# Kernel tuning notes

Measured on AMD Instinct MI355X. Metric: run time of the kernel, lower is better.

Reference implementation:

```python
import jax, jax.numpy as jnp
import numpy as np

B, S, D, H = 2, 2048, 2048, 16
HD = D // H
RESIDUAL_SCALE = 1.0
EPS = 1e-6


def setup_inputs() -> dict:
    key = jax.random.key(0)
    ks = jax.random.split(key, 6)
    x = jax.random.normal(ks[0], (B, S, D), jnp.float32)
    # rotary tables: emb = cat(freqs, freqs), shape [S, HD]
    inv_freq = 1.0 / (10000.0 ** (jnp.arange(0, HD, 2, dtype=jnp.float32) / HD))
    t = jnp.arange(S, dtype=jnp.float32)
    freqs = jnp.einsum('s,f->sf', t, inv_freq)
    emb = jnp.concatenate([freqs, freqs], axis=-1)
    cos, sin = jnp.cos(emb), jnp.sin(emb)
    sc = 0.02
    w_qkv = jax.random.normal(ks[1], (3 * D, D), jnp.float32) * sc
    w_out = jax.random.normal(ks[2], (D, D), jnp.float32) * sc
    w_fc1 = jax.random.normal(ks[3], (4 * D, D), jnp.float32) * sc
    w_fc2 = jax.random.normal(ks[4], (D, 4 * D), jnp.float32) * sc
    g1 = jnp.ones((D,), jnp.float32)
    g2 = jnp.ones((D,), jnp.float32)
    return {'x': x, 'cos': cos, 'sin': sin, 'g1': g1, 'g2': g2,
            'w_qkv': w_qkv, 'w_out': w_out, 'w_fc1': w_fc1, 'w_fc2': w_fc2}


def _rmsnorm(x, g):
    xf = x.astype(jnp.float32)
    norm = jnp.sqrt(jnp.mean(xf * xf, axis=-1, keepdims=True) + EPS)
    return g * (xf / norm)


def _rotate_half(x):
    x1, x2 = jnp.split(x, 2, axis=-1)
    return jnp.concatenate([-x2, x1], axis=-1)


def _rope(t, cos, sin):
    # t: [B, S, H, HD]; cos/sin: [S, HD]
    c = cos[None, :, None, :]
    s = sin[None, :, None, :]
    return t * c + _rotate_half(t) * s


def reference(x, cos, sin, g1, g2, w_qkv, w_out, w_fc1, w_fc2):
    b, s, d = x.shape
    x_skip = x
    h = _rmsnorm(x, g1)
    qkv = (h @ w_qkv.T).reshape(b, s, 3, H, HD)
    q = _rope(qkv[:, :, 0], cos, sin)
    k = _rope(qkv[:, :, 1], cos, sin)
    v = qkv[:, :, 2]  # rotary is identity on v
    scale = 1.0 / jnp.sqrt(jnp.asarray(HD, dtype=q.dtype))
    scores = jnp.einsum('bqhd,bkhd->bhqk', q, k) * scale
    causal = jnp.triu(jnp.ones((s, s), dtype=bool), k=1)
    scores = jnp.where(causal[None, None], -jnp.inf, scores)
    attn = jax.nn.softmax(scores, axis=-1)
    o = jnp.einsum('bhqk,bkhd->bqhd', attn, v).reshape(b, s, d)
    x = x_skip + RESIDUAL_SCALE * (o @ w_out.T)
    x_skip = x
    h = _rmsnorm(x, g2)
    h = jax.nn.gelu(h @ w_fc1.T, approximate=True) @ w_fc2.T
    return x_skip + RESIDUAL_SCALE * h
```

## Files before the change

kernel.cpp:

```cpp
#include <hip/hip_runtime.h>
#include <stdint.h>

typedef unsigned short u16;
typedef u16 u16x4 __attribute__((ext_vector_type(4)));
typedef u16 u16x8 __attribute__((ext_vector_type(8)));
typedef __bf16 bf16x8 __attribute__((ext_vector_type(8)));
typedef float f32x4 __attribute__((ext_vector_type(4)));
typedef float f32x16 __attribute__((ext_vector_type(16)));

#define MFMA16 __builtin_amdgcn_mfma_f32_16x16x32_bf16
#define MFMA32 __builtin_amdgcn_mfma_f32_32x32x16_bf16

static __device__ __forceinline__ float b2f(u16 u) {
    union { unsigned int i; float f; } v; v.i = ((unsigned int)u) << 16; return v.f;
}
static __device__ __forceinline__ u16 f2b(float f) {
    union { float f; unsigned int i; } v; v.f = f;
    unsigned int r = (v.i + 0x7fffu + ((v.i >> 16) & 1u)) >> 16;
    return (u16)r;
}
static __device__ __forceinline__ unsigned pk2(float lo, float hi) {
    union { __bf16 b[2]; unsigned u; } t;
    t.b[0] = (__bf16)lo; t.b[1] = (__bf16)hi; return t.u;
}
static __device__ __forceinline__ void gload_lds16(const void* g, void* l) {
    __builtin_amdgcn_global_load_lds((__attribute__((address_space(1))) void*)g,
                                     (__attribute__((address_space(3))) void*)l,
                                     16, 0, 0);
}

__global__ __launch_bounds__(256) void cvt_k(const float* __restrict__ in,
                                             u16* __restrict__ out, long n) {
    long i = ((long)blockIdx.x * 256 + threadIdx.x) * 4;
    if (i >= n) return;
    float4 v = *(const float4*)(in + i);
    u16x4 o; o[0] = f2b(v.x); o[1] = f2b(v.y); o[2] = f2b(v.z); o[3] = f2b(v.w);
    *(u16x4*)(out + i) = o;
}

__global__ __launch_bounds__(256) void addred_k(float* __restrict__ xout,
                                                const float* __restrict__ p0,
                                                const float* __restrict__ p1) {
    long i = ((long)blockIdx.x * 256 + threadIdx.x) * 4;
    float4 a = *(const float4*)(xout + i);
    float4 b = *(const float4*)(p0 + i);
    float4 c = *(const float4*)(p1 + i);
    a.x += b.x + c.x; a.y += b.y + c.y; a.z += b.z + c.z; a.w += b.w + c.w;
    *(float4*)(xout + i) = a;
}

__global__ __launch_bounds__(256) void addred2_k(float* __restrict__ xout,
                                                 const float* __restrict__ x,
                                                 const float* __restrict__ p0,
                                                 const float* __restrict__ p1) {
    long i = ((long)blockIdx.x * 256 + threadIdx.x) * 4;
    float4 r = *(const float4*)(x + i);
    float4 b = *(const float4*)(p0 + i);
    float4 c = *(const float4*)(p1 + i);
    r.x += b.x + c.x; r.y += b.y + c.y; r.z += b.z + c.z; r.w += b.w + c.w;
    *(float4*)(xout + i) = r;
}

__global__ __launch_bounds__(256) void rmsnorm_k(const float* __restrict__ x,
                                                 const float* __restrict__ g,
                                                 u16* __restrict__ out) {
    const long row = blockIdx.x;
    const int tid = threadIdx.x;
    const float* xr = x + row * 2048;
    float4 a = *(const float4*)(xr + tid * 4);
    float4 b = *(const float4*)(xr + 1024 + tid * 4);
    float ss = a.x*a.x + a.y*a.y + a.z*a.z + a.w*a.w
             + b.x*b.x + b.y*b.y + b.z*b.z + b.w*b.w;
    #pragma unroll
    for (int d = 1; d < 64; d <<= 1) ss += __shfl_xor(ss, d);
    __shared__ float red[4];
    if ((tid & 63) == 0) red[tid >> 6] = ss;
    __syncthreads();
    float tot = red[0] + red[1] + red[2] + red[3];
    float rinv = rsqrtf(tot * (1.0f / 2048.0f) + 1e-6f);
    float4 g0 = *(const float4*)(g + tid * 4);
    float4 g1 = *(const float4*)(g + 1024 + tid * 4);
    u16x4 o0, o1;
    o0[0] = f2b(a.x * g0.x * rinv); o0[1] = f2b(a.y * g0.y * rinv);
    o0[2] = f2b(a.z * g0.z * rinv); o0[3] = f2b(a.w * g0.w * rinv);
    o1[0] = f2b(b.x * g1.x * rinv); o1[1] = f2b(b.y * g1.y * rinv);
    o1[2] = f2b(b.z * g1.z * rinv); o1[3] = f2b(b.w * g1.w * rinv);
    *(u16x4*)(out + row * 2048 + tid * 4) = o0;
    *(u16x4*)(out + row * 2048 + 1024 + tid * 4) = o1;
}

__global__ __launch_bounds__(256) void rope_k(u16* __restrict__ qkv,
                                              const float* __restrict__ cosb,
                                              const float* __restrict__ sinb) {
    long idx = (long)blockIdx.x * 256 + threadIdx.x;
    int d = (int)(idx & 15) * 4;
    int h = (int)((idx >> 4) & 15);
    int which = (int)((idx >> 8) & 1);
    long row = idx >> 9;
    int s = (int)(row & 2047);
    u16* base = qkv + row * 6144 + which * 2048 + h * 128;
    u16x4 ua = *(u16x4*)(base + d);
    u16x4 ub = *(u16x4*)(base + d + 64);
    float4 c4 = *(const float4*)(cosb + (long)s * 128 + d);
    float4 s4 = *(const float4*)(sinb + (long)s * 128 + d);
    float cc[4] = {c4.x, c4.y, c4.z, c4.w};
    float sn[4] = {s4.x, s4.y, s4.z, s4.w};
    float scale = (which == 0) ? 0.08838834764831845f : 1.0f;
    u16x4 oa, ob;
    #pragma unroll
    for (int j = 0; j < 4; ++j) {
        float a = b2f(ua[j]), b = b2f(ub[j]);
        oa[j] = f2b((a * cc[j] - b * sn[j]) * scale);
        ob[j] = f2b((b * cc[j] + a * sn[j]) * scale);
    }
    *(u16x4*)(base + d) = oa;
    *(u16x4*)(base + d + 64) = ob;
}

__global__ __launch_bounds__(256) void vtrans_k(const u16* __restrict__ qkv,
                                                u16* __restrict__ vt) {
    __shared__ u16 t[128 * 65];
    const int bh = blockIdx.y, b = bh >> 4, h = bh & 15;
    const int s0 = blockIdx.x * 64;
    const int tid = threadIdx.x;
    #pragma unroll
    for (int it = 0; it < 4; ++it) {
        int flat = it * 256 + tid;
        int sl = flat >> 4, slot = flat & 15;
        u16x8 v = *(const u16x8*)(qkv + (long)(b * 2048 + s0 + sl) * 6144 + 4096 +
                                  h * 128 + slot * 8);
        #pragma unroll
        for (int j = 0; j < 8; ++j) t[(slot * 8 + j) * 65 + sl] = v[j];
    }
    __syncthreads();
    #pragma unroll
    for (int it = 0; it < 4; ++it) {
        int flat = it * 256 + tid;
        int d = flat >> 3, sg = flat & 7;
        u16x8 v;
        #pragma unroll
        for (int j = 0; j < 8; ++j) v[j] = t[d * 65 + sg * 8 + j];
        *(u16x8*)(vt + ((long)bh * 128 + d) * 2048 + s0 + sg * 8) = v;
    }
}

#define DS_A(BUF, SM, KK) (*(const bf16x8*)(ldsb + (BUF)*32768 + \
        ((((SM)*2) + (KK)) << 10) + rin64 + cst2))
#define DS_B(BUF, SN, KK) (*(const bf16x8*)(ldsb + 65536 + (BUF)*32768 + \
        ((((SN)*2) + (KK)) << 10) + rin64 + cst2))
#define STAGE_A(BUF, SK, KT) do { \
    gload_lds16(sA0 + ((long)(KT)*64 + (SK)*32), ldsb + (BUF)*32768 + (w4 + (SK))*1024); \
    gload_lds16(sA1 + ((long)(KT)*64 + (SK)*32), ldsb + (BUF)*32768 + (w4 + 2 + (SK))*1024); \
} while (0)
#define STAGE_B(BUF, SK, KT) do { \
    gload_lds16(sB0 + ((long)(KT)*64 + (SK)*32), ldsb + 65536 + (BUF)*32768 + (w4 + (SK))*1024); \
    gload_lds16(sB1 + ((long)(KT)*64 + (SK)*32), ldsb + 65536 + (BUF)*32768 + (w4 + 2 + (SK))*1024); \
} while (0)
#define PHASE(BUF, MH, KK, RDB, STAGE_STMT, VM) do { \
    bf16x8 af[4]; \
    _Pragma("unroll") \
    for (int m = 0; m < 4; ++m) af[m] = DS_A(BUF, wr8 + (MH)*4 + m, KK); \
    if (RDB) { \
        bfr[0] = DS_B(BUF, wc4 + 0, KK); bfr[1] = DS_B(BUF, wc4 + 1, KK); \
        bfr[2] = DS_B(BUF, wc4 + 2, KK); bfr[3] = DS_B(BUF, wc4 + 3, KK); \
    } \
    STAGE_STMT; \
    if (VM) { asm volatile("s_waitcnt vmcnt(6)" ::: "memory"); } \
    __builtin_amdgcn_sched_barrier(0); \
    __builtin_amdgcn_s_barrier(); \
    __builtin_amdgcn_sched_barrier(0); \
    __builtin_amdgcn_s_setprio(1); \
    _Pragma("unroll") \
    for (int m = 0; m < 4; ++m) \
        _Pragma("unroll") \
        for (int n = 0; n < 4; ++n) \
            acc[(MH)*4 + m][n] = MFMA16(af[m], bfr[n], acc[(MH)*4 + m][n], 0, 0, 0); \
    __builtin_amdgcn_s_setprio(0); \
    __builtin_amdgcn_sched_barrier(0); \
    __builtin_amdgcn_s_barrier(); \
    __builtin_amdgcn_sched_barrier(0); \
} while (0)

template <int EPI>
__global__ __launch_bounds__(512, 2) void gemm256(const u16* __restrict__ A,
                                                  const u16* __restrict__ W,
                                                  int M, int N, int K,
                                                  u16* outb, float* outf,
                                                  const float* res, int ksplit) {
    __shared__ u16 lds_[65536];
    char* ldsb = (char*)lds_;
    const int tid = threadIdx.x;
    const int w = tid >> 6, l = tid & 63;
    const int w4 = w * 4;
    const int wr8 = (w >> 2) * 8;
    const int wc4 = (w & 3) * 4;
    const int rin64 = (l & 15) * 64;
    const int cst2 = ((((l >> 4) * 8) ^ (((l >> 3) & 1) << 4)) << 1);

    const int nbn = N >> 8;
    const int nbm = M >> 8;
    const int nwg = gridDim.x;
    const int cpx = nwg >> 3;
    const int bid = blockIdx.x;
    int wg = (bid & 7) * cpx + (bid >> 3);
    int kseg = 0;
    int Keff = K;
    if (ksplit == 2) {
        kseg = wg & 1;
        wg >>= 1;
        Keff = K >> 1;
    }
    const int grp = 8 * nbn;
    const int g8 = wg / grp;
    const int rem = wg - g8 * grp;
    const int bm0 = g8 * 8;
    const int gmh = (nbm - bm0 < 8) ? (nbm - bm0) : 8;
    const int bn = rem / gmh;
    const int bm = bm0 + rem % gmh;
    const u16* Ab = A + (long)kseg * Keff;
    const u16* Wb = W + (long)kseg * Keff;

    const int r4 = l >> 2;
    const int clog = ((l & 3) * 8) ^ (((r4 >> 3) & 1) << 4);
    const u16* sA0 = Ab + ((long)bm * 256 + (w * 2 + 0) * 16 + r4) * K + clog;
    const u16* sA1 = Ab + ((long)bm * 256 + (w * 2 + 1) * 16 + r4) * K + clog;
    const u16* sB0 = Wb + ((long)bn * 256 + (w * 2 + 0) * 16 + r4) * K + clog;
    const u16* sB1 = Wb + ((long)bn * 256 + (w * 2 + 1) * 16 + r4) * K + clog;

    f32x4 acc[8][4];
    #pragma unroll
    for (int m = 0; m < 8; ++m)
        #pragma unroll
        for (int n = 0; n < 4; ++n) acc[m][n] = (f32x4){0.f, 0.f, 0.f, 0.f};
    bf16x8 bfr[4];

    const int nkt = Keff >> 6;
    const int niter = nkt >> 1;

    STAGE_B(0, 0, 0); STAGE_A(0, 0, 0); STAGE_B(0, 1, 0); STAGE_A(0, 1, 0);
    STAGE_B(1, 0, 1); STAGE_A(1, 0, 1); STAGE_B(1, 1, 1);
    asm volatile("s_waitcnt vmcnt(6)" ::: "memory");
    __builtin_amdgcn_sched_barrier(0);
    __builtin_amdgcn_s_barrier();
    __builtin_amdgcn_sched_barrier(0);

    for (int it = 0; it < niter; ++it) {
        const int t = it * 2;
        const int t1 = t + 1;
        const int t2 = (t + 2 < nkt) ? t + 2 : nkt - 1;
        const int t3 = (t + 3 < nkt) ? t + 3 : nkt - 1;
        PHASE(0, 0, 0, 1, STAGE_A(1, 1, t1), 0);
        PHASE(0, 1, 0, 0, STAGE_B(0, 0, t2), 0);
        PHASE(0, 0, 1, 1, STAGE_A(0, 0, t2), 0);
        PHASE(0, 1, 1, 0, STAGE_B(0, 1, t2), 1);
        PHASE(1, 0, 0, 1, STAGE_A(0, 1, t2), 0);
        PHASE(1, 1, 0, 0, STAGE_B(1, 0, t3), 0);
        PHASE(1, 0, 1, 1, STAGE_A(1, 0, t3), 0);
        PHASE(1, 1, 1, 0, STAGE_B(1, 1, t3), 1);
    }
    asm volatile("s_waitcnt vmcnt(0)" ::: "memory");

    const int rb = bm * 256 + (wr8 >> 3) * 128 + ((l >> 4) << 2);
    const int cb = bn * 256 + (w & 3) * 64 + (l & 15);
    float* pf = (EPI == 3) ? (outf + (long)kseg * M * N) : outf;
    #pragma unroll
    for (int m = 0; m < 8; ++m) {
        #pragma unroll
        for (int r = 0; r < 4; ++r) {
            long row = rb + m * 16 + r;
            #pragma unroll
            for (int n = 0; n < 4; ++n) {
                long col = cb + n * 16;
                float v = acc[m][n][r];
                if (EPI == 1) {
                    pf[row * N + col] = res[row * N + col] + v;
                } else if (EPI == 2) {
                    float u = 0.7978845608028654f * v * (1.0f + 0.044715f * v * v);
                    float e = __expf(2.0f * u);
                    float tgl = 1.0f - 2.0f / (e + 1.0f);
                    outb[row * N + col] = f2b(0.5f * v * (1.0f + tgl));
                } else if (EPI == 3) {
                    pf[row * N + col] = v;
                } else {
                    outb[row * N + col] = f2b(v);
                }
            }
        }
    }
}

struct AttnState {
    f32x16 acc[4];
    float m_i, l_i;
};

template <bool DIAG>
static __device__ __forceinline__ void attn_tile(
    int kv0, int qg, int wave, int l31, int hi,
    const u16* __restrict__ Ks, const u16* __restrict__ Vt,
    const bf16x8 (&qf)[8], AttnState& st)
{
    const bool do_g1 = !(DIAG && wave == 0);
    f32x16 sacc0, sacc1;
    #pragma unroll
    for (int r = 0; r < 16; ++r) { sacc0[r] = 0.f; sacc1[r] = 0.f; }

    #pragma unroll
    for (int dsl = 0; dsl < 8; ++dsl) {
        int slot = dsl * 2 + hi;
        int kv = l31;
        int sw = (slot & 8) | ((slot & 7) ^ (kv & 7));
        bf16x8 kf = *(const bf16x8*)(Ks + kv * 128 + sw * 8);
        sacc0 = MFMA32(kf, qf[dsl], sacc0, 0, 0, 0);
    }
    if (do_g1) {
        #pragma unroll
        for (int dsl = 0; dsl < 8; ++dsl) {
            int slot = dsl * 2 + hi;
            int kv = 32 + l31;
            int sw = (slot & 8) | ((slot & 7) ^ (kv & 7));
            bf16x8 kf = *(const bf16x8*)(Ks + kv * 128 + sw * 8);
            sacc1 = MFMA32(kf, qf[dsl], sacc1, 0, 0, 0);
        }
    }

    float sv[2][16];
    #pragma unroll
    for (int r = 0; r < 16; ++r) {
        sv[0][r] = sacc0[r];
        sv[1][r] = do_g1 ? sacc1[r] : -INFINITY;
    }
    if (DIAG) {
        #pragma unroll
        for (int g = 0; g < 2; ++g)
            #pragma unroll
            for (int r = 0; r < 16; ++r) {
                int kvg = kv0 + g * 32 + ((r & 3) + 8 * (r >> 2) + 4 * hi);
                if (kvg > qg) sv[g][r] = -INFINITY;
            }
    }

    float mx = sv[0][0];
    #pragma unroll
    for (int r = 1; r < 16; ++r) mx = fmaxf(mx, sv[0][r]);
    #pragma unroll
    for (int r = 0; r < 16; ++r) mx = fmaxf(mx, sv[1][r]);
    mx = fmaxf(mx, __shfl_xor(mx, 32));

    bool defer = __all(mx <= st.m_i + 8.0f);
    if (!defer) {
        float mnew = fmaxf(st.m_i, mx);
        float f = __expf(st.m_i - mnew);
        st.l_i *= f;
        #pragma unroll
        for (int dblk = 0; dblk < 4; ++dblk)
            #pragma unroll
            for (int r = 0; r < 16; ++r) st.acc[dblk][r] *= f;
        st.m_i = mnew;
    }

    float ssum = 0.f;
    #pragma unroll
    for (int g = 0; g < 2; ++g)
        #pragma unroll
        for (int r = 0; r < 16; ++r) {
            float e = __expf(sv[g][r] - st.m_i);
            sv[g][r] = e;
            ssum += e;
        }
    ssum += __shfl_xor(ssum, 32);
    st.l_i += ssum;

    unsigned w[2][4][2];
    #pragma unroll
    for (int g = 0; g < 2; ++g)
        #pragma unroll
        for (int q4 = 0; q4 < 4; ++q4) {
            w[g][q4][0] = pk2(sv[g][4 * q4 + 0], sv[g][4 * q4 + 1]);
            w[g][q4][1] = pk2(sv[g][4 * q4 + 2], sv[g][4 * q4 + 3]);
        }
    bf16x8 pfrag[4];
    #pragma unroll
    for (int ks = 0; ks < 4; ++ks) {
        int g = ks >> 1, h2 = ks & 1;
        unsigned o0 = hi ? w[g][2 * h2 + 1][0] : w[g][2 * h2][0];
        unsigned o1 = hi ? w[g][2 * h2 + 1][1] : w[g][2 * h2][1];
        unsigned t0 = hi ? w[g][2 * h2][0] : w[g][2 * h2 + 1][0];
        unsigned t1 = hi ? w[g][2 * h2][1] : w[g][2 * h2 + 1][1];
        unsigned s0v = __shfl_xor(t0, 32);
        unsigned s1v = __shfl_xor(t1, 32);
        union { unsigned u[4]; bf16x8 v; } cv;
        cv.u[0] = hi ? s0v : o0;
        cv.u[1] = hi ? s1v : o1;
        cv.u[2] = hi ? o0 : s0v;
        cv.u[3] = hi ? o1 : s1v;
        pfrag[ks] = cv.v;
    }

    #pragma unroll
    for (int dblk = 0; dblk < 4; ++dblk) {
        int d = dblk * 32 + l31;
        #pragma unroll
        for (int ks = 0; ks < 4; ++ks) {
            if (ks >= 2 && !do_g1) continue;
            int slot = ks * 2 + hi;
            bf16x8 vf = *(const bf16x8*)(Vt + d * 64 + (slot ^ (d & 7)) * 8);
            st.acc[dblk] = MFMA32(vf, pfrag[ks], st.acc[dblk], 0, 0, 0);
        }
    }
}

__global__ __launch_bounds__(128) void attn2_k(const u16* __restrict__ qkv,
                                               const u16* __restrict__ vt,
                                               u16* __restrict__ out) {
    const int bh = blockIdx.y;
    const int b = bh >> 4, h = bh & 15;
    const int qb = blockIdx.x;
    const int q0 = qb * 64;
    const int tid = threadIdx.x, wave = tid >> 6, lane = tid & 63;
    const int l31 = lane & 31, hi = lane >> 5;
    const int brow = b * 2048;
    __shared__ u16 Ks_lds[64 * 128];
    __shared__ u16 Vt_lds[128 * 64];

    bf16x8 qf[8];
    {
        const u16* qp = qkv + (long)(brow + q0 + wave * 32 + l31) * 6144 +
                        h * 128 + hi * 8;
        #pragma unroll
        for (int dsl = 0; dsl < 8; ++dsl) qf[dsl] = *(const bf16x8*)(qp + dsl * 16);
    }

    AttnState st;
    st.m_i = -INFINITY; st.l_i = 0.f;
    #pragma unroll
    for (int dblk = 0; dblk < 4; ++dblk)
        #pragma unroll
        for (int r = 0; r < 16; ++r) st.acc[dblk][r] = 0.f;

    const int qg = q0 + wave * 32 + l31;

    for (int t = 0; t <= qb; ++t) {
        const int kv0 = t * 64;
        __syncthreads();
        #pragma unroll
        for (int i = 0; i < 8; ++i) {
            int kv = wave * 32 + i * 4 + (lane >> 4);
            int slot = lane & 15;
            int sw = (slot & 8) | ((slot & 7) ^ (kv & 7));
            const u16* src = qkv + (long)(brow + kv0 + kv) * 6144 + 2048 +
                             h * 128 + sw * 8;
            gload_lds16(src, (char*)Ks_lds + (wave * 32 + i * 4) * 256);
        }
        #pragma unroll
        for (int i = 0; i < 8; ++i) {
            int d = wave * 64 + i * 8 + (lane >> 3);
            int slot = lane & 7;
            int sw = slot ^ (d & 7);
            const u16* src = vt + ((long)bh * 128 + d) * 2048 + kv0 + sw * 8;
            gload_lds16(src, (char*)Vt_lds + (wave * 64 + i * 8) * 128);
        }
        __syncthreads();
        if (t < qb)
            attn_tile<false>(kv0, qg, wave, l31, hi, Ks_lds, Vt_lds, qf, st);
        else
            attn_tile<true>(kv0, qg, wave, l31, hi, Ks_lds, Vt_lds, qf, st);
    }

    float inv = 1.0f / st.l_i;
    long orow = (long)(brow + q0 + wave * 32 + l31);
    #pragma unroll
    for (int dblk = 0; dblk < 4; ++dblk)
        #pragma unroll
        for (int rq = 0; rq < 4; ++rq) {
            u16x4 o4;
            #pragma unroll
            for (int m = 0; m < 4; ++m) o4[m] = f2b(st.acc[dblk][rq * 4 + m] * inv);
            int d = dblk * 32 + 8 * rq + 4 * hi;
            *(u16x4*)(out + orow * 2048 + h * 128 + d) = o4;
        }
}

extern "C" void kernel_launch(void* const* d_in, const int* in_sizes, int n_in,
                              void* d_out, int out_size, void* d_ws, size_t ws_size,
                              hipStream_t stream) {
    const float* x     = (const float*)d_in[0];
    const float* cosb  = (const float*)d_in[1];
    const float* sinb  = (const float*)d_in[2];
    const float* g1    = (const float*)d_in[3];
    const float* g2    = (const float*)d_in[4];
    const float* w_qkv = (const float*)d_in[5];
    const float* w_out = (const float*)d_in[6];
    const float* w_fc1 = (const float*)d_in[7];
    const float* w_fc2 = (const float*)d_in[8];

    char* ws = (char*)d_ws;
    u16* wqkv_b = (u16*)(ws);
    u16* wout_b = (u16*)(ws + 25165824);
    u16* wfc1_b = (u16*)(ws + 33554432);
    u16* wfc2_b = (u16*)(ws + 67108864);
    u16* h_b    = (u16*)(ws + 100663296);
    u16* qkv_b  = (u16*)(ws + 117440512);
    u16* attn_b = (u16*)(ws + 167772160);
    u16* vt_b   = h_b;
    u16* hg_b   = qkv_b;
    float* part = (float*)ws;
    float* pop  = (float*)(ws + 100663296);
    float* xout = (float*)d_out;

    cvt_k<<<12288, 256, 0, stream>>>(w_qkv, wqkv_b, 12582912L);
    cvt_k<<<4096, 256, 0, stream>>>(w_out, wout_b, 4194304L);
    cvt_k<<<16384, 256, 0, stream>>>(w_fc1, wfc1_b, 16777216L);
    cvt_k<<<16384, 256, 0, stream>>>(w_fc2, wfc2_b, 16777216L);

    rmsnorm_k<<<4096, 256, 0, stream>>>(x, g1, h_b);
    gemm256<0><<<384, 512, 0, stream>>>(h_b, wqkv_b, 4096, 6144, 2048,
                                        qkv_b, nullptr, nullptr, 1);
    rope_k<<<8192, 256, 0, stream>>>(qkv_b, cosb, sinb);
    vtrans_k<<<dim3(32, 32), 256, 0, stream>>>(qkv_b, vt_b);
    attn2_k<<<dim3(32, 32), 128, 0, stream>>>(qkv_b, vt_b, attn_b);
    gemm256<3><<<256, 512, 0, stream>>>(attn_b, wout_b, 4096, 2048, 2048,
                                        nullptr, pop, nullptr, 2);
    addred2_k<<<8192, 256, 0, stream>>>(xout, x, pop, pop + 8388608);
    rmsnorm_k<<<4096, 256, 0, stream>>>(xout, g2, h_b);
    gemm256<2><<<512, 512, 0, stream>>>(h_b, wfc1_b, 4096, 8192, 2048,
                                        hg_b, nullptr, nullptr, 1);
    gemm256<3><<<256, 512, 0, stream>>>(hg_b, wfc2_b, 4096, 2048, 8192,
                                        nullptr, part, nullptr, 2);
    addred_k<<<8192, 256, 0, stream>>>(xout, part, part + 8388608);
}
```

Measured before the change: 677.0 us.

## Double-buffer attention KV tiles with 128-row Q blocks and fuse residual-add into RMSNorm

The attention kernel now uses 4 waves per block covering 128 query rows. It double-buffers the K and V^T tiles in LDS, prefetching the next tile while the current one is computed, with a partial vmcnt wait between them. Causal masking is decided per wave from the row offset, so waves whose rows are entirely above a tile skip it. The post-attention residual add and the second RMSNorm are fused into one kernel, which saves a launch and a full read/write of the fp32 hidden state. The costs are twice the LDS per block and possible load imbalance, since some waves idle on the diagonal tiles.

```diff
diff --git a/kernel.cpp b/kernel.cpp
--- a/kernel.cpp
+++ b/kernel.cpp
@@ -49,16 +49,44 @@
     *(float4*)(xout + i) = a;
 }
 
-__global__ __launch_bounds__(256) void addred2_k(float* __restrict__ xout,
-                                                 const float* __restrict__ x,
-                                                 const float* __restrict__ p0,
-                                                 const float* __restrict__ p1) {
-    long i = ((long)blockIdx.x * 256 + threadIdx.x) * 4;
-    float4 r = *(const float4*)(x + i);
-    float4 b = *(const float4*)(p0 + i);
-    float4 c = *(const float4*)(p1 + i);
-    r.x += b.x + c.x; r.y += b.y + c.y; r.z += b.z + c.z; r.w += b.w + c.w;
-    *(float4*)(xout + i) = r;
+__global__ __launch_bounds__(256) void addrednorm_k(float* __restrict__ xout,
+                                                    const float* __restrict__ x,
+                                                    const float* __restrict__ p0,
+                                                    const float* __restrict__ p1,
+                                                    const float* __restrict__ g,
+                                                    u16* __restrict__ out) {
+    const long row = blockIdx.x;
+    const int tid = threadIdx.x;
+    const long base = row * 2048;
+    float4 a = *(const float4*)(x + base + tid * 4);
+    float4 b = *(const float4*)(p0 + base + tid * 4);
+    float4 c = *(const float4*)(p1 + base + tid * 4);
+    a.x += b.x + c.x; a.y += b.y + c.y; a.z += b.z + c.z; a.w += b.w + c.w;
+    float4 a2 = *(const float4*)(x + base + 1024 + tid * 4);
+    float4 b2 = *(const float4*)(p0 + base + 1024 + tid * 4);
+    float4 c2 = *(const float4*)(p1 + base + 1024 + tid * 4);
+    a2.x += b2.x + c2.x; a2.y += b2.y + c2.y;
+    a2.z += b2.z + c2.z; a2.w += b2.w + c2.w;
+    *(float4*)(xout + base + tid * 4) = a;
+    *(float4*)(xout + base + 1024 + tid * 4) = a2;
+    float ss = a.x*a.x + a.y*a.y + a.z*a.z + a.w*a.w
+             + a2.x*a2.x + a2.y*a2.y + a2.z*a2.z + a2.w*a2.w;
+    #pragma unroll
+    for (int d = 1; d < 64; d <<= 1) ss += __shfl_xor(ss, d);
+    __shared__ float red[4];
+    if ((tid & 63) == 0) red[tid >> 6] = ss;
+    __syncthreads();
+    float tot = red[0] + red[1] + red[2] + red[3];
+    float rinv = rsqrtf(tot * (1.0f / 2048.0f) + 1e-6f);
+    float4 g0 = *(const float4*)(g + tid * 4);
+    float4 g1 = *(const float4*)(g + 1024 + tid * 4);
+    u16x4 o0, o1;
+    o0[0] = f2b(a.x * g0.x * rinv); o0[1] = f2b(a.y * g0.y * rinv);
+    o0[2] = f2b(a.z * g0.z * rinv); o0[3] = f2b(a.w * g0.w * rinv);
+    o1[0] = f2b(a2.x * g1.x * rinv); o1[1] = f2b(a2.y * g1.y * rinv);
+    o1[2] = f2b(a2.z * g1.z * rinv); o1[3] = f2b(a2.w * g1.w * rinv);
+    *(u16x4*)(out + base + tid * 4) = o0;
+    *(u16x4*)(out + base + 1024 + tid * 4) = o1;
 }
 
 __global__ __launch_bounds__(256) void rmsnorm_k(const float* __restrict__ x,
@@ -296,11 +324,10 @@
 
 template <bool DIAG>
 static __device__ __forceinline__ void attn_tile(
-    int kv0, int qg, int wave, int l31, int hi,
+    int kv0, int qg, bool do_g1, int l31, int hi,
     const u16* __restrict__ Ks, const u16* __restrict__ Vt,
     const bf16x8 (&qf)[8], AttnState& st)
 {
-    const bool do_g1 = !(DIAG && wave == 0);
     f32x16 sacc0, sacc1;
     #pragma unroll
     for (int r = 0; r < 16; ++r) { sacc0[r] = 0.f; sacc1[r] = 0.f; }
@@ -410,18 +437,23 @@
     }
 }
 
-__global__ __launch_bounds__(128) void attn2_k(const u16* __restrict__ qkv,
+__global__ __launch_bounds__(256) void attn3_k(const u16* __restrict__ qkv,
                                                const u16* __restrict__ vt,
                                                u16* __restrict__ out) {
     const int bh = blockIdx.y;
     const int b = bh >> 4, h = bh & 15;
     const int qb = blockIdx.x;
-    const int q0 = qb * 64;
+    const int q0 = qb * 128;
     const int tid = threadIdx.x, wave = tid >> 6, lane = tid & 63;
     const int l31 = lane & 31, hi = lane >> 5;
     const int brow = b * 2048;
-    __shared__ u16 Ks_lds[64 * 128];
-    __shared__ u16 Vt_lds[128 * 64];
+    __shared__ u16 Ks_lds[2][64 * 128];
+    __shared__ u16 Vt_lds[2][128 * 64];
+
+    const int krow = tid >> 4;
+    const int kslot = tid & 15;
+    const int vrow = tid >> 3;
+    const int vslot = tid & 7;
 
     bf16x8 qf[8];
     {
@@ -438,34 +470,56 @@
         #pragma unroll
         for (int r = 0; r < 16; ++r) st.acc[dblk][r] = 0.f;
 
-    const int qg = q0 + wave * 32 + l31;
-
-    for (int t = 0; t <= qb; ++t) {
+    const int r0 = q0 + wave * 32;
+    const int qg = r0 + l31;
+    const int nt = 2 * qb + 2;
+    int cur = 0;
+
+#define STAGE_KV(BUF, KV0) do { \
+    _Pragma("unroll") \
+    for (int i = 0; i < 4; ++i) { \
+        int kv = i * 16 + krow; \
+        int sw = (kslot & 8) | ((kslot & 7) ^ (kv & 7)); \
+        const u16* src = qkv + (long)(brow + (KV0) + kv) * 6144 + 2048 + \
+                         h * 128 + sw * 8; \
+        gload_lds16(src, (char*)Ks_lds[BUF] + (i * 16 + wave * 4) * 256); \
+    } \
+    _Pragma("unroll") \
+    for (int i = 0; i < 4; ++i) { \
+        int d = i * 32 + vrow; \
+        int sw = vslot ^ (d & 7); \
+        const u16* src = vt + ((long)bh * 128 + d) * 2048 + (KV0) + sw * 8; \
+        gload_lds16(src, (char*)Vt_lds[BUF] + (i * 32 + wave * 8) * 128); \
+    } \
+} while (0)
+
+    STAGE_KV(0, 0);
+    for (int t = 0; t < nt; ++t) {
         const int kv0 = t * 64;
-        __syncthreads();
-        #pragma unroll
-        for (int i = 0; i < 8; ++i) {
-            int kv = wave * 32 + i * 4 + (lane >> 4);
-            int slot = lane & 15;
-            int sw = (slot & 8) | ((slot & 7) ^ (kv & 7));
-            const u16* src = qkv + (long)(brow + kv0 + kv) * 6144 + 2048 +
-                             h * 128 + sw * 8;
-            gload_lds16(src, (char*)Ks_lds + (wave * 32 + i * 4) * 256);
-        }
-        #pragma unroll
-        for (int i = 0; i < 8; ++i) {
-            int d = wave * 64 + i * 8 + (lane >> 3);
-            int slot = lane & 7;
-            int sw = slot ^ (d & 7);
-            const u16* src = vt + ((long)bh * 128 + d) * 2048 + kv0 + sw * 8;
-            gload_lds16(src, (char*)Vt_lds + (wave * 64 + i * 8) * 128);
-        }
-        __syncthreads();
-        if (t < qb)
-            attn_tile<false>(kv0, qg, wave, l31, hi, Ks_lds, Vt_lds, qf, st);
-        else
-            attn_tile<true>(kv0, qg, wave, l31, hi, Ks_lds, Vt_lds, qf, st);
-    }
+        const bool more = (t + 1 < nt);
+        if (more) {
+            if (cur) STAGE_KV(0, kv0 + 64); else STAGE_KV(1, kv0 + 64);
+        }
+        if (more) { asm volatile("s_waitcnt vmcnt(8)" ::: "memory"); }
+        else      { asm volatile("s_waitcnt vmcnt(0)" ::: "memory"); }
+        __builtin_amdgcn_sched_barrier(0);
+        __builtin_amdgcn_s_barrier();
+        __builtin_amdgcn_sched_barrier(0);
+        {
+            const u16* Ks = Ks_lds[cur];
+            const u16* Vt_ = Vt_lds[cur];
+            const int delta = r0 - kv0;
+            if (delta >= 64)
+                attn_tile<false>(kv0, qg, true, l31, hi, Ks, Vt_, qf, st);
+            else if (delta >= 0)
+                attn_tile<true>(kv0, qg, delta >= 32, l31, hi, Ks, Vt_, qf, st);
+        }
+        __builtin_amdgcn_sched_barrier(0);
+        __builtin_amdgcn_s_barrier();
+        __builtin_amdgcn_sched_barrier(0);
+        cur ^= 1;
+    }
+#undef STAGE_KV
 
     float inv = 1.0f / st.l_i;
     long orow = (long)(brow + q0 + wave * 32 + l31);
@@ -518,11 +572,10 @@
                                         qkv_b, nullptr, nullptr, 1);
     rope_k<<<8192, 256, 0, stream>>>(qkv_b, cosb, sinb);
     vtrans_k<<<dim3(32, 32), 256, 0, stream>>>(qkv_b, vt_b);
-    attn2_k<<<dim3(32, 32), 128, 0, stream>>>(qkv_b, vt_b, attn_b);
+    attn3_k<<<dim3(16, 32), 256, 0, stream>>>(qkv_b, vt_b, attn_b);
     gemm256<3><<<256, 512, 0, stream>>>(attn_b, wout_b, 4096, 2048, 2048,
                                         nullptr, pop, nullptr, 2);
-    addred2_k<<<8192, 256, 0, stream>>>(xout, x, pop, pop + 8388608);
-    rmsnorm_k<<<4096, 256, 0, stream>>>(xout, g2, h_b);
+    addrednorm_k<<<4096, 256, 0, stream>>>(xout, x, pop, pop + 8388608, g2, h_b);
     gemm256<2><<<512, 512, 0, stream>>>(h_b, wfc1_b, 4096, 8192, 2048,
                                         hg_b, nullptr, nullptr, 1);
     gemm256<3><<<256, 512, 0, stream>>>(hg_b, wfc2_b, 4096, 2048, 8192,
```

New measurement: 604.7 us. 10.7% less time.
